# Kernel tuning notes

Measured on AMD Instinct MI355X. Metric: run time of the kernel, lower is better.

Reference implementation:

```python
import jax, jax.numpy as jnp
import numpy as np

B = 8192       # atmospheric columns (batch)
NLAY = 60      # vertical levels (RNN sequence length)
NX = 4         # per-level input features
NXS = 3        # surface scalar inputs
NH1 = 64       # rnn1 hidden
NH2 = 64       # rnn2 hidden
NMEM = 16      # latent memory width (nh_mem)
NY = 4         # per-level outputs
NYS = 3        # surface outputs


def _lstm(x, h0, c0, Wih, Whh, bih, bhh):
    """PyTorch-convention LSTM (gate order i,f,g,o). x: [B,T,nx] -> ([B,T,nh], hL, cL)."""
    b = bih + bhh
    WihT = Wih.T
    WhhT = Whh.T

    def step(carry, xt):
        h, c = carry
        g = xt @ WihT + h @ WhhT + b
        i, f, gg, o = jnp.split(g, 4, axis=-1)
        c = jax.nn.sigmoid(f) * c + jax.nn.sigmoid(i) * jnp.tanh(gg)
        h = jax.nn.sigmoid(o) * jnp.tanh(c)
        return (h, c), h

    (hL, cL), ys = jax.lax.scan(step, (h0, c0), jnp.swapaxes(x, 0, 1))
    return jnp.swapaxes(ys, 0, 1), hL, cL


def setup_inputs() -> dict:
    key = jax.random.key(0)
    ks = jax.random.split(key, 30)

    def p(i, shape):
        return jax.random.normal(ks[i], shape, jnp.float32) * 0.05

    return {
        "inputs_main": jax.random.normal(ks[0], (B, NLAY, NX), jnp.float32),
        "inputs_aux": jax.random.normal(ks[1], (B, NXS), jnp.float32),
        "rnn1_mem": jax.random.normal(ks[2], (B, NLAY, NMEM), jnp.float32),
        # mlp_initial: Linear(nx, nneur[0])
        "Wi": p(3, (NH1, NX)), "bi": p(4, (NH1,)),
        # mlp_surface1/2: Linear(nx_sfc, nh_rnn1)
        "Ws1": p(5, (NH1, NXS)), "bs1": p(6, (NH1,)),
        "Ws2": p(7, (NH1, NXS)), "bs2": p(8, (NH1,)),
        # mlp_toa1/2: Linear(1, nh_rnn2)
        "Wt1": p(9, (NH2, 1)), "bt1": p(10, (NH2,)),
        "Wt2": p(11, (NH2, 1)), "bt2": p(12, (NH2,)),
        # rnn1: LSTM(NH1+NMEM -> NH1)
        "Wih1": p(13, (4 * NH1, NH1 + NMEM)), "Whh1": p(14, (4 * NH1, NH1)),
        "bih1": p(15, (4 * NH1,)), "bhh1": p(16, (4 * NH1,)),
        # rnn2: LSTM(NH1 -> NH2)
        "Wih2": p(17, (4 * NH2, NH1)), "Whh2": p(18, (4 * NH2, NH2)),
        "bih2": p(19, (4 * NH2,)), "bhh2": p(20, (4 * NH2,)),
        # mlp_latent: Linear(NH2, NMEM)
        "Wl": p(21, (NMEM, NH2)), "bl": p(22, (NMEM,)),
        # mlp_output: Linear(NMEM, NY)
        "Wo": p(23, (NY, NMEM)), "bo": p(24, (NY,)),
        # mlp_surface_output: Linear(NH2, NYS)
        "Wso": p(25, (NYS, NH2)), "bso": p(26, (NYS,)),
    }


def reference(inputs_main, inputs_aux, rnn1_mem, Wi, bi, Ws1, bs1, Ws2, bs2,
              Wt1, bt1, Wt2, bt2, Wih1, Whh1, bih1, bhh1, Wih2, Whh2, bih2, bhh2,
              Wl, bl, Wo, bo, Wso, bso):
    # initial MLP + tanh
    x = jnp.tanh(inputs_main @ Wi.T + bi)                       # [B,L,NH1]
    # concat convective memory
    x = jnp.concatenate([x, rnn1_mem], axis=2)                  # [B,L,NH1+NMEM]
    # rnn1 runs surface->TOA: flip level axis
    x = jnp.flip(x, axis=1)
    hx = jnp.tanh(inputs_aux @ Ws1.T + bs1)                     # surface-conditioned h0
    cx = jnp.tanh(inputs_aux @ Ws2.T + bs2)
    r1, _, _ = _lstm(x, hx, cx, Wih1, Whh1, bih1, bhh1)
    r1 = jnp.flip(r1, axis=1)                                   # back to TOA->surface
    # rnn2 initialized from TOA scalar
    toa = inputs_aux[:, 1:2]
    hx2 = toa @ Wt1.T + bt1
    cx2 = toa @ Wt2.T + bt2
    r2, hL, _ = _lstm(r1, hx2, cx2, Wih2, Whh2, bih2, bhh2)     # [B,L,NH2]
    # intermediate latent MLP -> new per-level memory
    lat = r2 @ Wl.T + bl                                        # [B,L,NMEM]
    new_mem = lat
    out = lat @ Wo.T + bo                                       # [B,L,NY]
    out_sfc = hL @ Wso.T + bso                                  # [B,NYS]
    return (out, out_sfc, new_mem)
```

## Files before the change

### kernel.cpp

```cpp
#include <hip/hip_runtime.h>
#include <hip/hip_bf16.h>

#define BATCH 8192
#define NLAY  60
#define NH    64
#define ROWS  16
#define TPB   256
#define S1    168
#define S2    136

typedef unsigned short ushort_t;
typedef __attribute__((ext_vector_type(8))) short short8;
typedef __attribute__((ext_vector_type(4))) float f32x4;
typedef __attribute__((ext_vector_type(4))) float f4v;

__device__ __forceinline__ float rcp_(float x) { return __builtin_amdgcn_rcpf(x); }
__device__ __forceinline__ float sigm_(float x) { return rcp_(1.0f + __expf(-x)); }
__device__ __forceinline__ float tanh_(float x) { return 1.0f - 2.0f * rcp_(__expf(2.0f * x) + 1.0f); }
__device__ __forceinline__ ushort_t f2bu(float f) {
  unsigned u = __float_as_uint(f);
  return (ushort_t)((u + 0x7FFFu + ((u >> 16) & 1u)) >> 16);
}
__device__ __forceinline__ unsigned pkbf(float a, float b) {
  union { __hip_bfloat162 h; unsigned u; } c;
  c.h = __float22bfloat162_rn(make_float2(a, b));
  return c.u;
}
__device__ __forceinline__ f32x4 mfma16(short8 a, short8 b, f32x4 c) {
  return __builtin_amdgcn_mfma_f32_16x16x32_bf16(a, b, c, 0, 0, 0);
}

__global__ void wtranspose(const float* __restrict__ Wih1, const float* __restrict__ Whh1,
                           const float* __restrict__ Wih2, const float* __restrict__ Whh2,
                           const float* __restrict__ Wl,   const float* __restrict__ Wo,
                           const float* __restrict__ Wso,  ushort_t* __restrict__ frag) {
  int e = blockIdx.x * 256 + threadIdx.x;
  float v;
  if (e < 40960) {
    int j = e & 7, lx = (e >> 3) & 63, rest = e >> 9;
    int ks = rest % 5, gw = rest / 5;
    int g = gw & 3, wv = gw >> 2;
    int uu = wv * 16 + (lx & 15);
    int k = ks * 32 + (lx >> 4) * 8 + j;
    int row = g * 64 + uu;
    v = (k < 80) ? Wih1[row * 80 + k] : (k < 144 ? Whh1[row * 64 + (k - 80)] : 0.0f);
  } else if (e < 73728) {
    int e2 = e - 40960;
    int j = e2 & 7, lx = (e2 >> 3) & 63, rest = e2 >> 9;
    int ks = rest & 3, g = (rest >> 2) & 3, wv = rest >> 4;
    int uu = wv * 16 + (lx & 15);
    int k = ks * 32 + (lx >> 4) * 8 + j;
    int row = g * 64 + uu;
    v = (k < 64) ? Wih2[row * 64 + k] : Whh2[row * 64 + (k - 64)];
  } else if (e < 74752) {
    int e3 = e - 73728;
    int j = e3 & 7, lx = (e3 >> 3) & 63, ks = e3 >> 9;
    int n = lx & 15, k = ks * 32 + (lx >> 4) * 8 + j;
    v = Wl[n * 64 + k];
  } else if (e < 75776) {
    int e4 = e - 74752;
    int j = e4 & 7, lx = (e4 >> 3) & 63, ks = e4 >> 9;
    int n = lx & 15, k = ks * 32 + (lx >> 4) * 8 + j;
    v = 0.0f;
    if (n < 4) {
#pragma unroll
      for (int m = 0; m < 16; ++m) v += Wo[n * 16 + m] * Wl[m * 64 + k];
    }
  } else {
    int e5 = e - 75776;
    int j = e5 & 7, lx = (e5 >> 3) & 63, ks = e5 >> 9;
    int n = lx & 15, k = ks * 32 + (lx >> 4) * 8 + j;
    v = (n < 3) ? Wso[n * 64 + k] : 0.0f;
  }
  frag[e] = f2bu(v);
}

__global__ __launch_bounds__(TPB, 2)
void lstm_fused(const float* __restrict__ inputs_main, const float* __restrict__ inputs_aux,
                const float* __restrict__ rnn1_mem,
                const float* __restrict__ Wi,  const float* __restrict__ bi,
                const float* __restrict__ Ws1, const float* __restrict__ bs1,
                const float* __restrict__ Ws2, const float* __restrict__ bs2,
                const float* __restrict__ Wt1, const float* __restrict__ bt1,
                const float* __restrict__ Wt2, const float* __restrict__ bt2,
                const float* __restrict__ bih1, const float* __restrict__ bhh1,
                const float* __restrict__ bih2, const float* __restrict__ bhh2,
                const float* __restrict__ bl,  const float* __restrict__ Wo,
                const float* __restrict__ bo,  const float* __restrict__ bso,
                const ushort_t* __restrict__ frag,
                ushort_t* __restrict__ r1buf,
                float* __restrict__ out, float* __restrict__ out_sfc,
                float* __restrict__ new_mem) {
  const ushort_t* W1f = frag;
  const ushort_t* W2f = frag + 40960;
  const ushort_t* WlF = frag + 73728;
  const ushort_t* WcF = frag + 74752;
  const ushort_t* WsF = frag + 75776;

  __shared__ __align__(16) ushort_t xh1[2][16 * S1];
  __shared__ __align__(16) ushort_t xh2[2][16 * S2];
  __shared__ __align__(16) float inmS[16][244];

  const int tid = threadIdx.x;
  const int l  = tid & 63, w = tid >> 6;
  const int ln = l & 15,  lq = l >> 4;
  const int u  = w * 16 + ln;
  const int rowbase = lq * 4;
  const int b0 = blockIdx.x * ROWS;
  const int xr = tid >> 4, xm = tid & 15, xc0 = xm * 4;
  const int rr8 = tid >> 3, ch8 = tid & 7;

  short8 B1f[4][5];
#pragma unroll
  for (int g = 0; g < 4; ++g)
#pragma unroll
    for (int ks = 0; ks < 5; ++ks)
      B1f[g][ks] = *(const short8*)(W1f + (((w * 4 + g) * 5 + ks) << 9) + (l << 3));

  f4v wif[4];
#pragma unroll
  for (int cc = 0; cc < 4; ++cc) wif[cc] = *(const f4v*)(Wi + (xc0 + cc) * 4);
  f4v bifv = *(const f4v*)(bi + xc0);

  float bg1[4];
#pragma unroll
  for (int g = 0; g < 4; ++g) bg1[g] = bih1[g * 64 + u] + bhh1[g * 64 + u];

  for (int e = tid; e < 16 * 240; e += TPB) {
    int r = e / 240, c = e - r * 240;
    inmS[r][c] = inputs_main[(size_t)(b0 + r) * 240 + c];
  }
  {
    int r = tid >> 4, c = 144 + (tid & 15);
    xh1[0][r * S1 + c] = 0; xh1[1][r * S1 + c] = 0;
  }
  __syncthreads();

  float c1[4];
  {
    float mv = rnn1_mem[(size_t)(b0 + xr) * 960 + 59 * 16 + xm];
    xh1[0][xr * S1 + 64 + xm] = f2bu(mv);
    f4v xin = *(const f4v*)&inmS[xr][59 * 4];
    float xp[4];
#pragma unroll
    for (int cc = 0; cc < 4; ++cc)
      xp[cc] = tanh_(bifv[cc] + wif[cc][0]*xin[0] + wif[cc][1]*xin[1] + wif[cc][2]*xin[2] + wif[cc][3]*xin[3]);
    *(uint2*)&xh1[0][xr * S1 + xc0] = make_uint2(pkbf(xp[0], xp[1]), pkbf(xp[2], xp[3]));

    float w10 = Ws1[u * 3 + 0], w11 = Ws1[u * 3 + 1], w12 = Ws1[u * 3 + 2], bb1 = bs1[u];
    float w20 = Ws2[u * 3 + 0], w21 = Ws2[u * 3 + 1], w22 = Ws2[u * 3 + 2], bb2 = bs2[u];
#pragma unroll
    for (int reg = 0; reg < 4; ++reg) {
      int row = rowbase + reg;
      const float* ax = inputs_aux + (size_t)(b0 + row) * 3;
      float a0 = ax[0], a1 = ax[1], a2 = ax[2];
      xh1[0][row * S1 + 80 + u] = f2bu(tanh_(w10 * a0 + w11 * a1 + w12 * a2 + bb1));
      c1[reg] = tanh_(w20 * a0 + w21 * a1 + w22 * a2 + bb2);
    }
  }
  __syncthreads();

  int pb = 0;
  for (int t = NLAY - 1; t >= 0; --t) {
    const int nb = pb ^ 1;
    float mv = 0.0f; f4v xin = {};
    if (t > 0) {
      mv  = rnn1_mem[(size_t)(b0 + xr) * 960 + (t - 1) * 16 + xm];
      xin = *(const f4v*)&inmS[xr][(t - 1) * 4];
    }
    short8 af[5];
#pragma unroll
    for (int ks = 0; ks < 5; ++ks)
      af[ks] = *(const short8*)&xh1[pb][ln * S1 + ks * 32 + lq * 8];

    f32x4 acc[4];
#pragma unroll
    for (int g = 0; g < 4; ++g) acc[g] = (f32x4){bg1[g], bg1[g], bg1[g], bg1[g]};
#pragma unroll
    for (int ks = 0; ks < 5; ++ks)
#pragma unroll
      for (int g = 0; g < 4; ++g) acc[g] = mfma16(af[ks], B1f[g][ks], acc[g]);

    if (t > 0) {
      float xp[4];
#pragma unroll
      for (int cc = 0; cc < 4; ++cc)
        xp[cc] = tanh_(bifv[cc] + wif[cc][0]*xin[0] + wif[cc][1]*xin[1] + wif[cc][2]*xin[2] + wif[cc][3]*xin[3]);
      *(uint2*)&xh1[nb][xr * S1 + xc0] = make_uint2(pkbf(xp[0], xp[1]), pkbf(xp[2], xp[3]));
      xh1[nb][xr * S1 + 64 + xm] = f2bu(mv);
    }

    float h[4];
#pragma unroll
    for (int reg = 0; reg < 4; ++reg) {
      float ig = sigm_(acc[0][reg]);
      float fg = sigm_(acc[1][reg]);
      float gg = tanh_(acc[2][reg]);
      float og = sigm_(acc[3][reg]);
      float c  = fg * c1[reg] + ig * gg;
      c1[reg] = c;
      h[reg] = og * tanh_(c);
    }
    unsigned h01 = pkbf(h[0], h[1]), h23 = pkbf(h[2], h[3]);
    ushort_t hu[4] = {(ushort_t)h01, (ushort_t)(h01 >> 16), (ushort_t)h23, (ushort_t)(h23 >> 16)};
#pragma unroll
    for (int reg = 0; reg < 4; ++reg) {
      r1buf[((size_t)(b0 + rowbase + reg) * 60 + t) * 64 + u] = hu[reg];
      if (t > 0) xh1[nb][(rowbase + reg) * S1 + 80 + u] = hu[reg];
      else       xh2[0][(rowbase + reg) * S2 + u]       = hu[reg];
    }
    __syncthreads();
    pb = nb;
  }

  short8 B2f[4][4];
#pragma unroll
  for (int g = 0; g < 4; ++g)
#pragma unroll
    for (int ks = 0; ks < 4; ++ks)
      B2f[g][ks] = *(const short8*)(W2f + (((w * 4 + g) * 4 + ks) << 9) + (l << 3));
  float bg2[4];
#pragma unroll
  for (int g = 0; g < 4; ++g) bg2[g] = bih2[g * 64 + u] + bhh2[g * 64 + u];

  float c2[4];
  {
    float wt1u = Wt1[u], wt2u = Wt2[u], bt1u = bt1[u], bt2u = bt2[u];
#pragma unroll
    for (int reg = 0; reg < 4; ++reg) {
      int row = rowbase + reg;
      float toa = inputs_aux[(size_t)(b0 + row) * 3 + 1];
      xh2[0][row * S2 + 64 + u] = f2bu(toa * wt1u + bt1u);
      c2[reg] = toa * wt2u + bt2u;
    }
  }
  short8 PW0 = {}, PW1 = {};
  float pbias = 0.0f;
  if (w == 0) {
    PW0 = *(const short8*)(WlF + (l << 3));
    PW1 = *(const short8*)(WlF + 512 + (l << 3));
    pbias = bl[ln];
  } else if (w == 1) {
    PW0 = *(const short8*)(WcF + (l << 3));
    PW1 = *(const short8*)(WcF + 512 + (l << 3));
    if (ln < 4) {
      float a = bo[ln];
#pragma unroll
      for (int m = 0; m < 16; ++m) a += Wo[ln * 16 + m] * bl[m];
      pbias = a;
    }
  } else if (w == 2) {
    PW0 = *(const short8*)(WsF + (l << 3));
    PW1 = *(const short8*)(WsF + 512 + (l << 3));
    pbias = (ln < 3) ? bso[ln] : 0.0f;
  }
  __syncthreads();

  pb = 0;
  for (int t = 0; t < NLAY; ++t) {
    const int nb = pb ^ 1;
    short8 r1v = {};
    if (t < 59 && tid < 128)
      r1v = *(const short8*)(r1buf + ((size_t)(b0 + rr8) * 60 + (t + 1)) * 64 + ch8 * 8);
    short8 af2[4];
#pragma unroll
    for (int ks = 0; ks < 4; ++ks)
      af2[ks] = *(const short8*)&xh2[pb][ln * S2 + ks * 32 + lq * 8];

    f32x4 acc[4];
#pragma unroll
    for (int g = 0; g < 4; ++g) acc[g] = (f32x4){bg2[g], bg2[g], bg2[g], bg2[g]};
#pragma unroll
    for (int ks = 0; ks < 4; ++ks)
#pragma unroll
      for (int g = 0; g < 4; ++g) acc[g] = mfma16(af2[ks], B2f[g][ks], acc[g]);

    if (t > 0 && w < 2) {
      short8 aL0 = *(const short8*)&xh2[pb][ln * S2 + 64 + lq * 8];
      short8 aL1 = *(const short8*)&xh2[pb][ln * S2 + 96 + lq * 8];
      f32x4 ap = (f32x4){pbias, pbias, pbias, pbias};
      ap = mfma16(aL0, PW0, ap);
      ap = mfma16(aL1, PW1, ap);
      if (w == 0) {
#pragma unroll
        for (int reg = 0; reg < 4; ++reg)
          new_mem[((size_t)(b0 + rowbase + reg) * 60 + (t - 1)) * 16 + ln] = ap[reg];
      } else if (ln < 4) {
#pragma unroll
        for (int reg = 0; reg < 4; ++reg)
          out[((size_t)(b0 + rowbase + reg) * 60 + (t - 1)) * 4 + ln] = ap[reg];
      }
    }

    float h[4];
#pragma unroll
    for (int reg = 0; reg < 4; ++reg) {
      float ig = sigm_(acc[0][reg]);
      float fg = sigm_(acc[1][reg]);
      float gg = tanh_(acc[2][reg]);
      float og = sigm_(acc[3][reg]);
      float c  = fg * c2[reg] + ig * gg;
      c2[reg] = c;
      h[reg] = og * tanh_(c);
    }
    unsigned h01 = pkbf(h[0], h[1]), h23 = pkbf(h[2], h[3]);
    ushort_t hu[4] = {(ushort_t)h01, (ushort_t)(h01 >> 16), (ushort_t)h23, (ushort_t)(h23 >> 16)};
#pragma unroll
    for (int reg = 0; reg < 4; ++reg)
      xh2[nb][(rowbase + reg) * S2 + 64 + u] = hu[reg];
    if (t < 59 && tid < 128)
      *(short8*)&xh2[nb][rr8 * S2 + ch8 * 8] = r1v;
    __syncthreads();
    pb = nb;
  }

  if (w < 3) {
    short8 aL0 = *(const short8*)&xh2[0][ln * S2 + 64 + lq * 8];
    short8 aL1 = *(const short8*)&xh2[0][ln * S2 + 96 + lq * 8];
    f32x4 ap = (f32x4){pbias, pbias, pbias, pbias};
    ap = mfma16(aL0, PW0, ap);
    ap = mfma16(aL1, PW1, ap);
    if (w == 0) {
#pragma unroll
      for (int reg = 0; reg < 4; ++reg)
        new_mem[((size_t)(b0 + rowbase + reg) * 60 + 59) * 16 + ln] = ap[reg];
    } else if (w == 1) {
      if (ln < 4) {
#pragma unroll
        for (int reg = 0; reg < 4; ++reg)
          out[((size_t)(b0 + rowbase + reg) * 60 + 59) * 4 + ln] = ap[reg];
      }
    } else {
      if (ln < 3) {
#pragma unroll
        for (int reg = 0; reg < 4; ++reg)
          out_sfc[(size_t)(b0 + rowbase + reg) * 3 + ln] = ap[reg];
      }
    }
  }
}

extern "C" void kernel_launch(void* const* d_in, const int* in_sizes, int n_in,
                              void* d_out, int out_size, void* d_ws, size_t ws_size,
                              hipStream_t stream) {
  (void)in_sizes; (void)n_in; (void)out_size; (void)ws_size;
  const float* inputs_main = (const float*)d_in[0];
  const float* inputs_aux  = (const float*)d_in[1];
  const float* rnn1_mem    = (const float*)d_in[2];
  const float* Wi   = (const float*)d_in[3];
  const float* bi   = (const float*)d_in[4];
  const float* Ws1  = (const float*)d_in[5];
  const float* bs1  = (const float*)d_in[6];
  const float* Ws2  = (const float*)d_in[7];
  const float* bs2  = (const float*)d_in[8];
  const float* Wt1  = (const float*)d_in[9];
  const float* bt1  = (const float*)d_in[10];
  const float* Wt2  = (const float*)d_in[11];
  const float* bt2  = (const float*)d_in[12];
  const float* Wih1 = (const float*)d_in[13];
  const float* Whh1 = (const float*)d_in[14];
  const float* bih1 = (const float*)d_in[15];
  const float* bhh1 = (const float*)d_in[16];
  const float* Wih2 = (const float*)d_in[17];
  const float* Whh2 = (const float*)d_in[18];
  const float* bih2 = (const float*)d_in[19];
  const float* bhh2 = (const float*)d_in[20];
  const float* Wl   = (const float*)d_in[21];
  const float* bl   = (const float*)d_in[22];
  const float* Wo   = (const float*)d_in[23];
  const float* bo   = (const float*)d_in[24];
  const float* Wso  = (const float*)d_in[25];
  const float* bso  = (const float*)d_in[26];

  float* out     = (float*)d_out;
  float* out_sfc = out + (size_t)BATCH * NLAY * 4;
  float* new_mem = out_sfc + (size_t)BATCH * 3;

  ushort_t* frag  = (ushort_t*)d_ws;
  ushort_t* r1buf = (ushort_t*)((char*)d_ws + 153600);

  wtranspose<<<300, 256, 0, stream>>>(Wih1, Whh1, Wih2, Whh2, Wl, Wo, Wso, frag);
  lstm_fused<<<BATCH / ROWS, TPB, 0, stream>>>(
      inputs_main, inputs_aux, rnn1_mem, Wi, bi, Ws1, bs1, Ws2, bs2,
      Wt1, bt1, Wt2, bt2, bih1, bhh1, bih2, bhh2, bl, Wo, bo, bso,
      frag, r1buf, out, out_sfc, new_mem);
}
```

Baseline: 263.5 us.

## Prescale LSTM weights by log2e, preload memory to LDS, block-local r1 layout, batched stores

Folds log2(e) and 2*log2(e) factors into the gate weights, biases and state so sigmoid/tanh use a raw exp2 without per-element multiplies. Preloads all rnn1_mem for the block into LDS as bf16 and reorders the K layout so the memory chunk is read directly as the fifth MFMA fragment, merging the two LSTM shared buffers into one. r1buf gets a per-block time-major layout, and rnn1 h writes to it are batched every four steps. The projection outputs (new_mem, out) are also buffered in registers and stored once per four-step group instead of every step, reusing the already-loaded A fragments. The extra LDS footprint may reduce occupancy, and the scaled cell state changes rounding slightly.

```diff
diff --git a/kernel.cpp b/kernel.cpp
--- a/kernel.cpp
+++ b/kernel.cpp
@@ -3,11 +3,13 @@
 
 #define BATCH 8192
 #define NLAY  60
-#define NH    64
 #define ROWS  16
 #define TPB   256
-#define S1    168
-#define S2    136
+#define SX    136
+#define SM    968
+#define SI    244
+#define LOG2E 1.44269504089f
+#define T2L   2.88539008178f
 
 typedef unsigned short ushort_t;
 typedef __attribute__((ext_vector_type(8))) short short8;
@@ -15,8 +17,7 @@
 typedef __attribute__((ext_vector_type(4))) float f4v;
 
 __device__ __forceinline__ float rcp_(float x) { return __builtin_amdgcn_rcpf(x); }
-__device__ __forceinline__ float sigm_(float x) { return rcp_(1.0f + __expf(-x)); }
-__device__ __forceinline__ float tanh_(float x) { return 1.0f - 2.0f * rcp_(__expf(2.0f * x) + 1.0f); }
+__device__ __forceinline__ float ex2_(float x) { return __builtin_amdgcn_exp2f(x); }
 __device__ __forceinline__ ushort_t f2bu(float f) {
   unsigned u = __float_as_uint(f);
   return (ushort_t)((u + 0x7FFFu + ((u >> 16) & 1u)) >> 16);
@@ -40,18 +41,21 @@
     int j = e & 7, lx = (e >> 3) & 63, rest = e >> 9;
     int ks = rest % 5, gw = rest / 5;
     int g = gw & 3, wv = gw >> 2;
-    int uu = wv * 16 + (lx & 15);
+    int row = g * 64 + wv * 16 + (lx & 15);
     int k = ks * 32 + (lx >> 4) * 8 + j;
-    int row = g * 64 + uu;
-    v = (k < 80) ? Wih1[row * 80 + k] : (k < 144 ? Whh1[row * 64 + (k - 80)] : 0.0f);
+    v = (k < 64)  ? Wih1[row * 80 + k]
+      : (k < 128) ? Whh1[row * 64 + (k - 64)]
+      : (k < 144) ? Wih1[row * 80 + 64 + (k - 128)]
+      : 0.0f;
+    v *= (g == 2) ? T2L : LOG2E;
   } else if (e < 73728) {
     int e2 = e - 40960;
     int j = e2 & 7, lx = (e2 >> 3) & 63, rest = e2 >> 9;
     int ks = rest & 3, g = (rest >> 2) & 3, wv = rest >> 4;
-    int uu = wv * 16 + (lx & 15);
+    int row = g * 64 + wv * 16 + (lx & 15);
     int k = ks * 32 + (lx >> 4) * 8 + j;
-    int row = g * 64 + uu;
     v = (k < 64) ? Wih2[row * 64 + k] : Whh2[row * 64 + (k - 64)];
+    v *= (g == 2) ? T2L : LOG2E;
   } else if (e < 74752) {
     int e3 = e - 73728;
     int j = e3 & 7, lx = (e3 >> 3) & 63, ks = e3 >> 9;
@@ -97,120 +101,153 @@
   const ushort_t* WcF = frag + 74752;
   const ushort_t* WsF = frag + 75776;
 
-  __shared__ __align__(16) ushort_t xh1[2][16 * S1];
-  __shared__ __align__(16) ushort_t xh2[2][16 * S2];
-  __shared__ __align__(16) float inmS[16][244];
+  __shared__ __align__(16) ushort_t xh[2][16 * SX];
+  __shared__ __align__(16) ushort_t memAll[16 * SM];
+  __shared__ __align__(16) float    inm[16 * SI];
 
   const int tid = threadIdx.x;
-  const int l  = tid & 63, w = tid >> 6;
-  const int ln = l & 15,  lq = l >> 4;
-  const int u  = w * 16 + ln;
+  const int lane = tid & 63, w = tid >> 6;
+  const int ln = lane & 15, lq = lane >> 4;
+  const int u = w * 16 + ln;
   const int rowbase = lq * 4;
   const int b0 = blockIdx.x * ROWS;
   const int xr = tid >> 4, xm = tid & 15, xc0 = xm * 4;
   const int rr8 = tid >> 3, ch8 = tid & 7;
 
+  ushort_t* r1blk = r1buf + (size_t)blockIdx.x * (60 * 16 * 64);
+
   short8 B1f[4][5];
 #pragma unroll
   for (int g = 0; g < 4; ++g)
 #pragma unroll
     for (int ks = 0; ks < 5; ++ks)
-      B1f[g][ks] = *(const short8*)(W1f + (((w * 4 + g) * 5 + ks) << 9) + (l << 3));
+      B1f[g][ks] = *(const short8*)(W1f + (((w * 4 + g) * 5 + ks) << 9) + (lane << 3));
+  float bg1[4];
+#pragma unroll
+  for (int g = 0; g < 4; ++g)
+    bg1[g] = (bih1[g * 64 + u] + bhh1[g * 64 + u]) * ((g == 2) ? T2L : LOG2E);
 
   f4v wif[4];
 #pragma unroll
-  for (int cc = 0; cc < 4; ++cc) wif[cc] = *(const f4v*)(Wi + (xc0 + cc) * 4);
-  f4v bifv = *(const f4v*)(bi + xc0);
-
-  float bg1[4];
-#pragma unroll
-  for (int g = 0; g < 4; ++g) bg1[g] = bih1[g * 64 + u] + bhh1[g * 64 + u];
+  for (int cc = 0; cc < 4; ++cc) wif[cc] = *(const f4v*)(Wi + (xc0 + cc) * 4) * T2L;
+  f4v bifv = *(const f4v*)(bi + xc0) * T2L;
 
   for (int e = tid; e < 16 * 240; e += TPB) {
     int r = e / 240, c = e - r * 240;
-    inmS[r][c] = inputs_main[(size_t)(b0 + r) * 240 + c];
-  }
+    inm[r * SI + c] = inputs_main[(size_t)(b0 + r) * 240 + c];
+  }
+  for (int e = tid; e < 16 * 960; e += TPB) {
+    int r = e / 960, c = e - r * 960;
+    memAll[r * SM + c] = f2bu(rnn1_mem[(size_t)(b0 + r) * 960 + c]);
+  }
+  __syncthreads();
+
+  float ct1[4];
   {
-    int r = tid >> 4, c = 144 + (tid & 15);
-    xh1[0][r * S1 + c] = 0; xh1[1][r * S1 + c] = 0;
-  }
-  __syncthreads();
-
-  float c1[4];
-  {
-    float mv = rnn1_mem[(size_t)(b0 + xr) * 960 + 59 * 16 + xm];
-    xh1[0][xr * S1 + 64 + xm] = f2bu(mv);
-    f4v xin = *(const f4v*)&inmS[xr][59 * 4];
+    f4v xin = *(const f4v*)&inm[xr * SI + 59 * 4];
     float xp[4];
 #pragma unroll
-    for (int cc = 0; cc < 4; ++cc)
-      xp[cc] = tanh_(bifv[cc] + wif[cc][0]*xin[0] + wif[cc][1]*xin[1] + wif[cc][2]*xin[2] + wif[cc][3]*xin[3]);
-    *(uint2*)&xh1[0][xr * S1 + xc0] = make_uint2(pkbf(xp[0], xp[1]), pkbf(xp[2], xp[3]));
-
-    float w10 = Ws1[u * 3 + 0], w11 = Ws1[u * 3 + 1], w12 = Ws1[u * 3 + 2], bb1 = bs1[u];
-    float w20 = Ws2[u * 3 + 0], w21 = Ws2[u * 3 + 1], w22 = Ws2[u * 3 + 2], bb2 = bs2[u];
+    for (int cc = 0; cc < 4; ++cc) {
+      float a = fmaf(wif[cc][3], xin[3], fmaf(wif[cc][2], xin[2],
+                fmaf(wif[cc][1], xin[1], fmaf(wif[cc][0], xin[0], bifv[cc]))));
+      xp[cc] = fmaf(rcp_(1.0f + ex2_(a)), -2.0f, 1.0f);
+    }
+    *(uint2*)&xh[0][xr * SX + xc0] = make_uint2(pkbf(xp[0], xp[1]), pkbf(xp[2], xp[3]));
+
+    float w10 = Ws1[u * 3 + 0] * T2L, w11 = Ws1[u * 3 + 1] * T2L, w12 = Ws1[u * 3 + 2] * T2L;
+    float bb1 = bs1[u] * T2L;
+    float w20 = Ws2[u * 3 + 0] * T2L, w21 = Ws2[u * 3 + 1] * T2L, w22 = Ws2[u * 3 + 2] * T2L;
+    float bb2 = bs2[u] * T2L;
 #pragma unroll
     for (int reg = 0; reg < 4; ++reg) {
       int row = rowbase + reg;
       const float* ax = inputs_aux + (size_t)(b0 + row) * 3;
       float a0 = ax[0], a1 = ax[1], a2 = ax[2];
-      xh1[0][row * S1 + 80 + u] = f2bu(tanh_(w10 * a0 + w11 * a1 + w12 * a2 + bb1));
-      c1[reg] = tanh_(w20 * a0 + w21 * a1 + w22 * a2 + bb2);
+      float ha = w10 * a0 + w11 * a1 + w12 * a2 + bb1;
+      xh[0][row * SX + 64 + u] = f2bu(fmaf(rcp_(1.0f + ex2_(ha)), -2.0f, 1.0f));
+      float ca = w20 * a0 + w21 * a1 + w22 * a2 + bb2;
+      ct1[reg] = fmaf(rcp_(1.0f + ex2_(ca)), -2.0f * T2L, T2L);
     }
   }
   __syncthreads();
 
+  ushort_t* r1t = r1blk + rowbase * 64 + u;
+  unsigned sxv[4], syv[4];
   int pb = 0;
-  for (int t = NLAY - 1; t >= 0; --t) {
-    const int nb = pb ^ 1;
-    float mv = 0.0f; f4v xin = {};
-    if (t > 0) {
-      mv  = rnn1_mem[(size_t)(b0 + xr) * 960 + (t - 1) * 16 + xm];
-      xin = *(const f4v*)&inmS[xr][(t - 1) * 4];
-    }
-    short8 af[5];
-#pragma unroll
-    for (int ks = 0; ks < 5; ++ks)
-      af[ks] = *(const short8*)&xh1[pb][ln * S1 + ks * 32 + lq * 8];
-
-    f32x4 acc[4];
-#pragma unroll
-    for (int g = 0; g < 4; ++g) acc[g] = (f32x4){bg1[g], bg1[g], bg1[g], bg1[g]};
-#pragma unroll
-    for (int ks = 0; ks < 5; ++ks)
-#pragma unroll
-      for (int g = 0; g < 4; ++g) acc[g] = mfma16(af[ks], B1f[g][ks], acc[g]);
-
-    if (t > 0) {
-      float xp[4];
-#pragma unroll
-      for (int cc = 0; cc < 4; ++cc)
-        xp[cc] = tanh_(bifv[cc] + wif[cc][0]*xin[0] + wif[cc][1]*xin[1] + wif[cc][2]*xin[2] + wif[cc][3]*xin[3]);
-      *(uint2*)&xh1[nb][xr * S1 + xc0] = make_uint2(pkbf(xp[0], xp[1]), pkbf(xp[2], xp[3]));
-      xh1[nb][xr * S1 + 64 + xm] = f2bu(mv);
-    }
-
-    float h[4];
-#pragma unroll
-    for (int reg = 0; reg < 4; ++reg) {
-      float ig = sigm_(acc[0][reg]);
-      float fg = sigm_(acc[1][reg]);
-      float gg = tanh_(acc[2][reg]);
-      float og = sigm_(acc[3][reg]);
-      float c  = fg * c1[reg] + ig * gg;
-      c1[reg] = c;
-      h[reg] = og * tanh_(c);
-    }
-    unsigned h01 = pkbf(h[0], h[1]), h23 = pkbf(h[2], h[3]);
-    ushort_t hu[4] = {(ushort_t)h01, (ushort_t)(h01 >> 16), (ushort_t)h23, (ushort_t)(h23 >> 16)};
-#pragma unroll
-    for (int reg = 0; reg < 4; ++reg) {
-      r1buf[((size_t)(b0 + rowbase + reg) * 60 + t) * 64 + u] = hu[reg];
-      if (t > 0) xh1[nb][(rowbase + reg) * S1 + 80 + u] = hu[reg];
-      else       xh2[0][(rowbase + reg) * S2 + u]       = hu[reg];
-    }
-    __syncthreads();
-    pb = nb;
+
+  for (int tg = 14; tg >= 0; --tg) {
+#pragma unroll
+    for (int s = 3; s >= 0; --s) {
+      const int t = tg * 4 + s;
+      const int nb = pb ^ 1;
+      const ushort_t* xrow = &xh[pb][ln * SX];
+      short8 af0 = *(const short8*)(xrow + lq * 8);
+      short8 af1 = *(const short8*)(xrow + 32 + lq * 8);
+      short8 af2 = *(const short8*)(xrow + 64 + lq * 8);
+      short8 af3 = *(const short8*)(xrow + 96 + lq * 8);
+      short8 af4 = {};
+      if (lq < 2) af4 = *(const short8*)(memAll + ln * SM + t * 16 + lq * 8);
+
+      f32x4 acc[4];
+#pragma unroll
+      for (int g = 0; g < 4; ++g) acc[g] = (f32x4){bg1[g], bg1[g], bg1[g], bg1[g]};
+#pragma unroll
+      for (int g = 0; g < 4; ++g) {
+        acc[g] = mfma16(af0, B1f[g][0], acc[g]);
+        acc[g] = mfma16(af1, B1f[g][1], acc[g]);
+        acc[g] = mfma16(af2, B1f[g][2], acc[g]);
+        acc[g] = mfma16(af3, B1f[g][3], acc[g]);
+        acc[g] = mfma16(af4, B1f[g][4], acc[g]);
+      }
+
+      if (t > 0) {
+        f4v xin = *(const f4v*)&inm[xr * SI + (t - 1) * 4];
+        float xp[4];
+#pragma unroll
+        for (int cc = 0; cc < 4; ++cc) {
+          float a = fmaf(wif[cc][3], xin[3], fmaf(wif[cc][2], xin[2],
+                    fmaf(wif[cc][1], xin[1], fmaf(wif[cc][0], xin[0], bifv[cc]))));
+          xp[cc] = fmaf(rcp_(1.0f + ex2_(a)), -2.0f, 1.0f);
+        }
+        *(uint2*)&xh[nb][xr * SX + xc0] = make_uint2(pkbf(xp[0], xp[1]), pkbf(xp[2], xp[3]));
+      }
+
+      float h[4];
+#pragma unroll
+      for (int reg = 0; reg < 4; ++reg) {
+        float si = rcp_(1.0f + ex2_(-acc[0][reg]));
+        float sf = rcp_(1.0f + ex2_(-acc[1][reg]));
+        float so = rcp_(1.0f + ex2_(-acc[3][reg]));
+        float gt = fmaf(rcp_(1.0f + ex2_(acc[2][reg])), -2.0f * T2L, T2L);
+        ct1[reg] = fmaf(sf, ct1[reg], si * gt);
+        float tc = fmaf(rcp_(1.0f + ex2_(ct1[reg])), -2.0f, 1.0f);
+        h[reg] = so * tc;
+      }
+      unsigned h01 = pkbf(h[0], h[1]), h23 = pkbf(h[2], h[3]);
+      sxv[s] = h01; syv[s] = h23;
+      if (t > 0) {
+        xh[nb][(rowbase + 0) * SX + 64 + u] = (ushort_t)h01;
+        xh[nb][(rowbase + 1) * SX + 64 + u] = (ushort_t)(h01 >> 16);
+        xh[nb][(rowbase + 2) * SX + 64 + u] = (ushort_t)h23;
+        xh[nb][(rowbase + 3) * SX + 64 + u] = (ushort_t)(h23 >> 16);
+      } else {
+        xh[nb][(rowbase + 0) * SX + u] = (ushort_t)h01;
+        xh[nb][(rowbase + 1) * SX + u] = (ushort_t)(h01 >> 16);
+        xh[nb][(rowbase + 2) * SX + u] = (ushort_t)h23;
+        xh[nb][(rowbase + 3) * SX + u] = (ushort_t)(h23 >> 16);
+      }
+      __syncthreads();
+      pb = nb;
+    }
+    ushort_t* rp = r1t + (tg << 12);
+#pragma unroll
+    for (int s = 0; s < 4; ++s) {
+      unsigned a = sxv[s], b = syv[s];
+      rp[s * 1024 + 0 * 64] = (ushort_t)a;
+      rp[s * 1024 + 1 * 64] = (ushort_t)(a >> 16);
+      rp[s * 1024 + 2 * 64] = (ushort_t)b;
+      rp[s * 1024 + 3 * 64] = (ushort_t)(b >> 16);
+    }
   }
 
   short8 B2f[4][4];
@@ -218,31 +255,32 @@
   for (int g = 0; g < 4; ++g)
 #pragma unroll
     for (int ks = 0; ks < 4; ++ks)
-      B2f[g][ks] = *(const short8*)(W2f + (((w * 4 + g) * 4 + ks) << 9) + (l << 3));
+      B2f[g][ks] = *(const short8*)(W2f + (((w * 4 + g) * 4 + ks) << 9) + (lane << 3));
   float bg2[4];
 #pragma unroll
-  for (int g = 0; g < 4; ++g) bg2[g] = bih2[g * 64 + u] + bhh2[g * 64 + u];
-
-  float c2[4];
+  for (int g = 0; g < 4; ++g)
+    bg2[g] = (bih2[g * 64 + u] + bhh2[g * 64 + u]) * ((g == 2) ? T2L : LOG2E);
+
+  float ct2[4];
   {
     float wt1u = Wt1[u], wt2u = Wt2[u], bt1u = bt1[u], bt2u = bt2[u];
 #pragma unroll
     for (int reg = 0; reg < 4; ++reg) {
       int row = rowbase + reg;
       float toa = inputs_aux[(size_t)(b0 + row) * 3 + 1];
-      xh2[0][row * S2 + 64 + u] = f2bu(toa * wt1u + bt1u);
-      c2[reg] = toa * wt2u + bt2u;
+      xh[pb][row * SX + 64 + u] = f2bu(toa * wt1u + bt1u);
+      ct2[reg] = (toa * wt2u + bt2u) * T2L;
     }
   }
   short8 PW0 = {}, PW1 = {};
   float pbias = 0.0f;
   if (w == 0) {
-    PW0 = *(const short8*)(WlF + (l << 3));
-    PW1 = *(const short8*)(WlF + 512 + (l << 3));
+    PW0 = *(const short8*)(WlF + (lane << 3));
+    PW1 = *(const short8*)(WlF + 512 + (lane << 3));
     pbias = bl[ln];
   } else if (w == 1) {
-    PW0 = *(const short8*)(WcF + (l << 3));
-    PW1 = *(const short8*)(WcF + 512 + (l << 3));
+    PW0 = *(const short8*)(WcF + (lane << 3));
+    PW1 = *(const short8*)(WcF + 512 + (lane << 3));
     if (ln < 4) {
       float a = bo[ln];
 #pragma unroll
@@ -250,85 +288,101 @@
       pbias = a;
     }
   } else if (w == 2) {
-    PW0 = *(const short8*)(WsF + (l << 3));
-    PW1 = *(const short8*)(WsF + 512 + (l << 3));
+    PW0 = *(const short8*)(WsF + (lane << 3));
+    PW1 = *(const short8*)(WsF + 512 + (lane << 3));
     pbias = (ln < 3) ? bso[ln] : 0.0f;
   }
+  const ushort_t* r1rp = r1blk + 1024 + rr8 * 64 + ch8 * 8;
+  float* nmb = new_mem + (size_t)(b0 + rowbase) * 960 + ln;
+  float* outb = out + (size_t)(b0 + rowbase) * 240 + ln;
+  f32x4 pst[4];
   __syncthreads();
 
-  pb = 0;
-  for (int t = 0; t < NLAY; ++t) {
-    const int nb = pb ^ 1;
-    short8 r1v = {};
-    if (t < 59 && tid < 128)
-      r1v = *(const short8*)(r1buf + ((size_t)(b0 + rr8) * 60 + (t + 1)) * 64 + ch8 * 8);
-    short8 af2[4];
-#pragma unroll
-    for (int ks = 0; ks < 4; ++ks)
-      af2[ks] = *(const short8*)&xh2[pb][ln * S2 + ks * 32 + lq * 8];
-
-    f32x4 acc[4];
-#pragma unroll
-    for (int g = 0; g < 4; ++g) acc[g] = (f32x4){bg2[g], bg2[g], bg2[g], bg2[g]};
-#pragma unroll
-    for (int ks = 0; ks < 4; ++ks)
-#pragma unroll
-      for (int g = 0; g < 4; ++g) acc[g] = mfma16(af2[ks], B2f[g][ks], acc[g]);
-
-    if (t > 0 && w < 2) {
-      short8 aL0 = *(const short8*)&xh2[pb][ln * S2 + 64 + lq * 8];
-      short8 aL1 = *(const short8*)&xh2[pb][ln * S2 + 96 + lq * 8];
-      f32x4 ap = (f32x4){pbias, pbias, pbias, pbias};
-      ap = mfma16(aL0, PW0, ap);
-      ap = mfma16(aL1, PW1, ap);
-      if (w == 0) {
-#pragma unroll
-        for (int reg = 0; reg < 4; ++reg)
-          new_mem[((size_t)(b0 + rowbase + reg) * 60 + (t - 1)) * 16 + ln] = ap[reg];
-      } else if (ln < 4) {
-#pragma unroll
-        for (int reg = 0; reg < 4; ++reg)
-          out[((size_t)(b0 + rowbase + reg) * 60 + (t - 1)) * 4 + ln] = ap[reg];
-      }
-    }
-
-    float h[4];
-#pragma unroll
-    for (int reg = 0; reg < 4; ++reg) {
-      float ig = sigm_(acc[0][reg]);
-      float fg = sigm_(acc[1][reg]);
-      float gg = tanh_(acc[2][reg]);
-      float og = sigm_(acc[3][reg]);
-      float c  = fg * c2[reg] + ig * gg;
-      c2[reg] = c;
-      h[reg] = og * tanh_(c);
-    }
-    unsigned h01 = pkbf(h[0], h[1]), h23 = pkbf(h[2], h[3]);
-    ushort_t hu[4] = {(ushort_t)h01, (ushort_t)(h01 >> 16), (ushort_t)h23, (ushort_t)(h23 >> 16)};
-#pragma unroll
-    for (int reg = 0; reg < 4; ++reg)
-      xh2[nb][(rowbase + reg) * S2 + 64 + u] = hu[reg];
-    if (t < 59 && tid < 128)
-      *(short8*)&xh2[nb][rr8 * S2 + ch8 * 8] = r1v;
-    __syncthreads();
-    pb = nb;
+  for (int tg = 0; tg < 15; ++tg) {
+#pragma unroll
+    for (int s = 0; s < 4; ++s) {
+      const int t = tg * 4 + s;
+      const int nb = pb ^ 1;
+      short8 r1v = {};
+      if (t < 59 && tid < 128) r1v = *(const short8*)(r1rp + t * 1024);
+
+      const ushort_t* xrow = &xh[pb][ln * SX];
+      short8 af0 = *(const short8*)(xrow + lq * 8);
+      short8 af1 = *(const short8*)(xrow + 32 + lq * 8);
+      short8 af2 = *(const short8*)(xrow + 64 + lq * 8);
+      short8 af3 = *(const short8*)(xrow + 96 + lq * 8);
+
+      f32x4 acc[4];
+#pragma unroll
+      for (int g = 0; g < 4; ++g) acc[g] = (f32x4){bg2[g], bg2[g], bg2[g], bg2[g]};
+#pragma unroll
+      for (int g = 0; g < 4; ++g) {
+        acc[g] = mfma16(af0, B2f[g][0], acc[g]);
+        acc[g] = mfma16(af1, B2f[g][1], acc[g]);
+        acc[g] = mfma16(af2, B2f[g][2], acc[g]);
+        acc[g] = mfma16(af3, B2f[g][3], acc[g]);
+      }
+
+      if (t > 0 && w < 2) {
+        f32x4 ap = (f32x4){pbias, pbias, pbias, pbias};
+        ap = mfma16(af2, PW0, ap);
+        ap = mfma16(af3, PW1, ap);
+        pst[(t - 1) & 3] = ap;
+      }
+
+      float h[4];
+#pragma unroll
+      for (int reg = 0; reg < 4; ++reg) {
+        float si = rcp_(1.0f + ex2_(-acc[0][reg]));
+        float sf = rcp_(1.0f + ex2_(-acc[1][reg]));
+        float so = rcp_(1.0f + ex2_(-acc[3][reg]));
+        float gt = fmaf(rcp_(1.0f + ex2_(acc[2][reg])), -2.0f * T2L, T2L);
+        ct2[reg] = fmaf(sf, ct2[reg], si * gt);
+        float tc = fmaf(rcp_(1.0f + ex2_(ct2[reg])), -2.0f, 1.0f);
+        h[reg] = so * tc;
+      }
+      unsigned h01 = pkbf(h[0], h[1]), h23 = pkbf(h[2], h[3]);
+      xh[nb][(rowbase + 0) * SX + 64 + u] = (ushort_t)h01;
+      xh[nb][(rowbase + 1) * SX + 64 + u] = (ushort_t)(h01 >> 16);
+      xh[nb][(rowbase + 2) * SX + 64 + u] = (ushort_t)h23;
+      xh[nb][(rowbase + 3) * SX + 64 + u] = (ushort_t)(h23 >> 16);
+      if (t < 59 && tid < 128)
+        *(short8*)&xh[nb][rr8 * SX + ch8 * 8] = r1v;
+      __syncthreads();
+      pb = nb;
+    }
+    if (w < 2) {
+      const int base = tg * 4;
+#pragma unroll
+      for (int k = 0; k < 4; ++k) {
+        const int pt = (k == 3) ? base - 1 : base + k;
+        if (pt < 0) continue;
+        f32x4 ap = pst[k];
+        if (w == 0) {
+#pragma unroll
+          for (int reg = 0; reg < 4; ++reg) nmb[reg * 960 + pt * 16] = ap[reg];
+        } else if (ln < 4) {
+#pragma unroll
+          for (int reg = 0; reg < 4; ++reg) outb[reg * 240 + pt * 4] = ap[reg];
+        }
+      }
+    }
   }
 
   if (w < 3) {
-    short8 aL0 = *(const short8*)&xh2[0][ln * S2 + 64 + lq * 8];
-    short8 aL1 = *(const short8*)&xh2[0][ln * S2 + 96 + lq * 8];
+    const ushort_t* xrow = &xh[pb][ln * SX];
+    short8 aL0 = *(const short8*)(xrow + 64 + lq * 8);
+    short8 aL1 = *(const short8*)(xrow + 96 + lq * 8);
     f32x4 ap = (f32x4){pbias, pbias, pbias, pbias};
     ap = mfma16(aL0, PW0, ap);
     ap = mfma16(aL1, PW1, ap);
     if (w == 0) {
 #pragma unroll
-      for (int reg = 0; reg < 4; ++reg)
-        new_mem[((size_t)(b0 + rowbase + reg) * 60 + 59) * 16 + ln] = ap[reg];
+      for (int reg = 0; reg < 4; ++reg) nmb[reg * 960 + 59 * 16] = ap[reg];
     } else if (w == 1) {
       if (ln < 4) {
 #pragma unroll
-        for (int reg = 0; reg < 4; ++reg)
-          out[((size_t)(b0 + rowbase + reg) * 60 + 59) * 4 + ln] = ap[reg];
+        for (int reg = 0; reg < 4; ++reg) outb[reg * 240 + 59 * 4] = ap[reg];
       }
     } else {
       if (ln < 3) {
```

After: 256.7 us. 2.6% less time.
